# Optimization experiments

Hardware: AMD Instinct MI355X
Metric: run time of the kernel (lower is better)

Reference implementation:

```python
import jax, jax.numpy as jnp
import numpy as np

H = 768
NH = 12
HD = H // NH
FF = 3072
EPS = 1e-12
SCALE = 1.0 / (HD ** 0.5)


def _ln(x, g, b):
    m = jnp.mean(x, axis=-1, keepdims=True)
    v = jnp.mean((x - m) ** 2, axis=-1, keepdims=True)
    return (x - m) * jax.lax.rsqrt(v + EPS) * g + b


def setup_inputs() -> dict:
    key = jax.random.key(0)
    ks = jax.random.split(key, 16)
    B, Q, S, T = 8, 64, 48, 128
    s = 0.02
    return {
        "q": jax.random.normal(ks[0], (B, Q, H), jnp.float32),
        "k": jax.random.normal(ks[1], (B, S, T, H), jnp.float32),
        "mask": jax.random.randint(ks[2], (B, S, T), 0, 2, jnp.int32),
        "Wq": jax.random.normal(ks[3], (H, H), jnp.float32) * s,
        "Wkv": jax.random.normal(ks[4], (H, H), jnp.float32) * s,
        "Wo": jax.random.normal(ks[5], (H, H), jnp.float32) * s,
        "bo": jnp.zeros((H,), jnp.float32),
        "ln1_g": jnp.ones((H,), jnp.float32),
        "ln1_b": jnp.zeros((H,), jnp.float32),
        "W1": jax.random.normal(ks[6], (H, FF), jnp.float32) * s,
        "b1": jnp.zeros((FF,), jnp.float32),
        "W2": jax.random.normal(ks[7], (FF, H), jnp.float32) * s,
        "b2": jnp.zeros((H,), jnp.float32),
        "ln2_g": jnp.ones((H,), jnp.float32),
        "ln2_b": jnp.zeros((H,), jnp.float32),
    }


def reference(q, k, mask, Wq, Wkv, Wo, bo, ln1_g, ln1_b, W1, b1, W2, b2, ln2_g, ln2_b):
    B, Q, _ = q.shape
    _, S, T, _ = k.shape
    # projections (no bias)
    qp = (q @ Wq).reshape(B, Q, NH, HD)            # [b,q,h,d]
    kv = (k @ Wkv).reshape(B, S, T, NH, HD)        # [b,s,t,h,d]
    # broadcast-query grouped attention: softmax only over token dim t
    scores = jnp.einsum('bqhd,bsthd->bhqst', qp, kv) * SCALE
    scores = scores + mask.astype(scores.dtype)[:, None, None, :, :] * -10000.0
    alpha = jax.nn.softmax(scores, axis=-1)        # dropout is identity in eval
    res = jnp.einsum('bhqst,bsthd->bqshd', alpha, kv).reshape(B, Q, S, H)
    # BertSelfOutput with zero residual (residual=False)
    attn_out = _ln(res @ Wo + bo, ln1_g, ln1_b)    # [b,q,s,H]
    # FFN
    ffn = jax.nn.gelu(attn_out @ W1 + b1, approximate=False) @ W2 + b2
    return _ln(attn_out + ffn, ln2_g, ln2_b)
```

## Files before the change

### kernel.cpp

```cpp
#include <hip/hip_runtime.h>
#include <hip/hip_bf16.h>
#include <math.h>

#define B_ 8
#define Q_ 64
#define S_ 48
#define T_ 128
#define H_ 768
#define NH_ 12
#define HD_ 64
#define FF_ 3072

typedef float f32x4 __attribute__((ext_vector_type(4)));
typedef short s16x8 __attribute__((ext_vector_type(8)));
typedef short s16x4 __attribute__((ext_vector_type(4)));

__device__ __forceinline__ float ldT(const float* p, size_t i) { return p[i]; }
__device__ __forceinline__ float ldT(const __hip_bfloat16* p, size_t i) { return __bfloat162float(p[i]); }
__device__ __forceinline__ void stT(float* p, size_t i, float v) { p[i] = v; }
__device__ __forceinline__ void stT(__hip_bfloat16* p, size_t i, float v) { p[i] = __float2bfloat16(v); }

__device__ __forceinline__ short f2bf(float f) {
  __hip_bfloat16 h = __float2bfloat16(f);
  return *reinterpret_cast<short*>(&h);
}

__device__ __forceinline__ float gelu_f(float x) {
  float z = 1.5957691216f * (x + 0.044715f * x * x * x);
  z = fminf(z, 80.0f);
  float e = __expf(z);
  return x * e / (e + 1.0f);
}

__device__ __forceinline__ void gld_lds16(const void* g, void* l) {
  __builtin_amdgcn_global_load_lds(
      (const __attribute__((address_space(1))) void*)g,
      (__attribute__((address_space(3))) void*)l, 16, 0, 0);
}

__device__ __forceinline__ int swz_off(int row, int kc) {
  return row * 64 + ((kc ^ ((row >> 1) & 3)) << 4);
}

#define WAITV4() asm volatile("s_waitcnt vmcnt(4)" ::: "memory")
#define WAITV5() asm volatile("s_waitcnt vmcnt(5)" ::: "memory")
#define WAITV0() asm volatile("s_waitcnt vmcnt(0)" ::: "memory")
#define BARX()   do { __builtin_amdgcn_s_barrier(); asm volatile("" ::: "memory"); } while (0)

template<int KK, typename OT, bool BIAS, bool GELU>
__global__ __launch_bounds__(256) void gemm_mfma(
    const __hip_bfloat16* __restrict__ A,
    const __hip_bfloat16* __restrict__ BT,
    const float* __restrict__ bias, OT* __restrict__ C,
    int N, int nbx, int GB)
{
  constexpr int NT = KK / 32;
  static_assert(NT % 3 == 0 && NT >= 6, "KK must be multiple of 96");
  __shared__ char sm[3][16384];

  const int cpx = gridDim.x >> 3;
  const int xcd = blockIdx.x & 7;
  const int ci  = blockIdx.x >> 3;
  const int gsz = GB * nbx;
  const int g   = ci / gsz;
  const int r2  = ci - g * gsz;
  const int bn  = r2 / GB;
  const int bi  = r2 - bn * GB;
  const int bm  = xcd * (cpx / nbx) + g * GB + bi;
  const int m0 = bm * 128, n0 = bn * 128;

  const int tid = threadIdx.x;
  const int lane = tid & 63;
  const int wid = tid >> 6;
  const int wr = wid >> 1, wc = wid & 1;
  const int kcg = lane >> 4, rl = lane & 15;

  const __hip_bfloat16* pA[2];
  const __hip_bfloat16* pB[2];
  #pragma unroll
  for (int r = 0; r < 2; ++r) {
    const int c = tid + r * 256, row = c >> 2, slot = c & 3;
    const int kc = slot ^ ((row >> 1) & 3);
    pA[r] = A + (size_t)(m0 + row) * KK + kc * 8;
    pB[r] = BT + (size_t)(n0 + row) * KK + kc * 8;
  }
  auto stageT = [&](char* base, int off) {
    gld_lds16(pA[0] + off, base + tid * 16);
    gld_lds16(pA[1] + off, base + tid * 16 + 4096);
    gld_lds16(pB[0] + off, base + 8192 + tid * 16);
    gld_lds16(pB[1] + off, base + 8192 + tid * 16 + 4096);
  };

  int woffA[4], woffB[4];
  #pragma unroll
  for (int m = 0; m < 4; ++m)
    woffA[m] = swz_off(wr * 64 + m * 16 + rl, kcg);
  #pragma unroll
  for (int n = 0; n < 4; ++n)
    woffB[n] = 8192 + swz_off(wc * 64 + n * 16 + rl, kcg);

  f32x4 acc[4][4] = {};
  s16x8 af[4], bf[4];
  auto reads = [&](const char* base) {
    #pragma unroll
    for (int m = 0; m < 4; ++m) af[m] = *(const s16x8*)(base + woffA[m]);
    #pragma unroll
    for (int n = 0; n < 4; ++n) bf[n] = *(const s16x8*)(base + woffB[n]);
  };
  auto mfmas = [&]() {
    #pragma unroll
    for (int m = 0; m < 4; ++m)
      #pragma unroll
      for (int n = 0; n < 4; ++n)
        acc[m][n] = __builtin_amdgcn_mfma_f32_16x16x32_bf16(af[m], bf[n], acc[m][n], 0, 0, 0);
  };

  stageT(sm[0], 0);
  stageT(sm[1], 32);
  #pragma unroll
  for (int r = 0; r < 2; ++r) { pA[r] += 64; pB[r] += 64; }

  #pragma unroll 1
  for (int it = 0; it < NT / 3 - 1; ++it) {
    WAITV4(); BARX(); reads(sm[0]); stageT(sm[2], 0);  mfmas();
    WAITV4(); BARX(); reads(sm[1]); stageT(sm[0], 32); mfmas();
    WAITV4(); BARX(); reads(sm[2]); stageT(sm[1], 64); mfmas();
    #pragma unroll
    for (int r = 0; r < 2; ++r) { pA[r] += 96; pB[r] += 96; }
  }
  WAITV4(); BARX(); reads(sm[0]); stageT(sm[2], 0); mfmas();
  WAITV4(); BARX(); reads(sm[1]); mfmas();
  WAITV0(); BARX(); reads(sm[2]); mfmas();

  const int colb = n0 + wc * 64 + rl;
  const int rowb = m0 + wr * 64 + (lane >> 4) * 4;
  float bv[4];
  #pragma unroll
  for (int n = 0; n < 4; ++n) bv[n] = BIAS ? bias[colb + n * 16] : 0.0f;
  #pragma unroll
  for (int m = 0; m < 4; ++m) {
    #pragma unroll
    for (int r = 0; r < 4; ++r) {
      const int row = rowb + m * 16 + r;
      #pragma unroll
      for (int n = 0; n < 4; ++n) {
        float v = acc[m][n][r] + bv[n];
        if (GELU) v = gelu_f(v);
        stT(C, (size_t)row * N + colb + n * 16, v);
      }
    }
  }
}

template<int KK, typename OT, bool BIAS, bool GELU>
__global__ __launch_bounds__(256, 2) void gemm_fat(
    const __hip_bfloat16* __restrict__ A,
    const __hip_bfloat16* __restrict__ BT,
    const float* __restrict__ bias, OT* __restrict__ C,
    int N, int nbx, int GB)
{
  constexpr int NT = KK / 32;
  static_assert(NT % 3 == 0 && NT >= 6, "KK must be multiple of 96");
  __shared__ char sm[3][20480];

  const int cpx = gridDim.x >> 3;
  const int xcd = blockIdx.x & 7;
  const int ci  = blockIdx.x >> 3;
  const int gsz = GB * nbx;
  const int g   = ci / gsz;
  const int r2  = ci - g * gsz;
  const int bn  = r2 / GB;
  const int bi  = r2 - bn * GB;
  const int bm  = xcd * (cpx / nbx) + g * GB + bi;
  const int m0 = bm * 128, n0 = bn * 192;

  const int tid = threadIdx.x;
  const int lane = tid & 63;
  const int wid = tid >> 6;
  const int wm = wid >> 1;
  const int wn = wid & 1;
  const int kcg = lane >> 4, rl = lane & 15;

  const __hip_bfloat16* pA[2];
  const __hip_bfloat16* pB[3];
  #pragma unroll
  for (int r = 0; r < 2; ++r) {
    const int c = tid + r * 256, row = c >> 2, slot = c & 3;
    const int kc = slot ^ ((row >> 1) & 3);
    pA[r] = A + (size_t)(m0 + row) * KK + kc * 8;
  }
  #pragma unroll
  for (int r = 0; r < 3; ++r) {
    const int c = tid + r * 256, row = c >> 2, slot = c & 3;
    const int kc = slot ^ ((row >> 1) & 3);
    pB[r] = BT + (size_t)(n0 + row) * KK + kc * 8;
  }
  auto stageT = [&](char* base, int off) {
    gld_lds16(pA[0] + off, base + tid * 16);
    gld_lds16(pA[1] + off, base + tid * 16 + 4096);
    gld_lds16(pB[0] + off, base + 8192 + tid * 16);
    gld_lds16(pB[1] + off, base + 8192 + tid * 16 + 4096);
    gld_lds16(pB[2] + off, base + 8192 + tid * 16 + 8192);
  };

  int woffA[4], woffB[6];
  #pragma unroll
  for (int m = 0; m < 4; ++m)
    woffA[m] = swz_off(wm * 64 + m * 16 + rl, kcg);
  #pragma unroll
  for (int n = 0; n < 6; ++n)
    woffB[n] = 8192 + swz_off(wn * 96 + n * 16 + rl, kcg);

  f32x4 acc[4][6] = {};
  s16x8 af[4], bf[6];
  auto reads = [&](const char* base) {
    #pragma unroll
    for (int m = 0; m < 4; ++m) af[m] = *(const s16x8*)(base + woffA[m]);
    #pragma unroll
    for (int n = 0; n < 6; ++n) bf[n] = *(const s16x8*)(base + woffB[n]);
  };
  auto mfmas = [&]() {
    #pragma unroll
    for (int m = 0; m < 4; ++m)
      #pragma unroll
      for (int n = 0; n < 6; ++n)
        acc[m][n] = __builtin_amdgcn_mfma_f32_16x16x32_bf16(af[m], bf[n], acc[m][n], 0, 0, 0);
  };

  stageT(sm[0], 0);
  stageT(sm[1], 32);
  #pragma unroll
  for (int r = 0; r < 2; ++r) pA[r] += 64;
  #pragma unroll
  for (int r = 0; r < 3; ++r) pB[r] += 64;

  #pragma unroll 1
  for (int it = 0; it < NT / 3 - 1; ++it) {
    WAITV5(); BARX(); reads(sm[0]); stageT(sm[2], 0);  mfmas();
    WAITV5(); BARX(); reads(sm[1]); stageT(sm[0], 32); mfmas();
    WAITV5(); BARX(); reads(sm[2]); stageT(sm[1], 64); mfmas();
    #pragma unroll
    for (int r = 0; r < 2; ++r) pA[r] += 96;
    #pragma unroll
    for (int r = 0; r < 3; ++r) pB[r] += 96;
  }
  WAITV5(); BARX(); reads(sm[0]); stageT(sm[2], 0); mfmas();
  WAITV5(); BARX(); reads(sm[1]); mfmas();
  WAITV0(); BARX(); reads(sm[2]); mfmas();

  const int colb = n0 + wn * 96 + rl;
  const int rowb = m0 + wm * 64 + (lane >> 4) * 4;
  float bv[6];
  #pragma unroll
  for (int n = 0; n < 6; ++n) bv[n] = BIAS ? bias[colb + n * 16] : 0.0f;
  #pragma unroll
  for (int m = 0; m < 4; ++m) {
    #pragma unroll
    for (int r = 0; r < 4; ++r) {
      const int row = rowb + m * 16 + r;
      #pragma unroll
      for (int n = 0; n < 6; ++n) {
        float v = acc[m][n][r] + bv[n];
        if (GELU) v = gelu_f(v);
        stT(C, (size_t)row * N + colb + n * 16, v);
      }
    }
  }
}

template<typename OT>
__global__ __launch_bounds__(256) void gemm64(
    const float* __restrict__ A, const float* __restrict__ W,
    OT* __restrict__ C, int M, int N, int K)
{
  __shared__ float As[16][65];
  __shared__ float Ws[16][65];
  const int tid = threadIdx.x;
  const int m0 = blockIdx.y * 64;
  const int n0 = blockIdx.x * 64;
  const int tx = (tid & 15) * 4;
  const int ty = (tid >> 4) * 4;
  float acc[4][4] = {};

  for (int k0 = 0; k0 < K; k0 += 16) {
    #pragma unroll
    for (int r = 0; r < 4; ++r) {
      int idx = tid + r * 256;
      int mm = idx >> 4, kk = idx & 15;
      As[kk][mm] = A[(size_t)(m0 + mm) * K + (k0 + kk)];
    }
    #pragma unroll
    for (int r = 0; r < 4; ++r) {
      int idx = tid + r * 256;
      int kk = idx >> 6, nn = idx & 63;
      Ws[kk][nn] = W[(size_t)(k0 + kk) * N + (n0 + nn)];
    }
    __syncthreads();
    #pragma unroll
    for (int kk = 0; kk < 16; ++kk) {
      float a[4], b[4];
      #pragma unroll
      for (int i = 0; i < 4; ++i) a[i] = As[kk][ty + i];
      #pragma unroll
      for (int j = 0; j < 4; ++j) b[j] = Ws[kk][tx + j];
      #pragma unroll
      for (int i = 0; i < 4; ++i)
        #pragma unroll
        for (int j = 0; j < 4; ++j) acc[i][j] += a[i] * b[j];
    }
    __syncthreads();
  }
  #pragma unroll
  for (int i = 0; i < 4; ++i)
    #pragma unroll
    for (int j = 0; j < 4; ++j)
      stT(C, (size_t)(m0 + ty + i) * N + (n0 + tx + j), acc[i][j]);
}

__global__ __launch_bounds__(256) void transpose_cast(
    const float* __restrict__ W, __hip_bfloat16* __restrict__ WT, int K, int N)
{
  __shared__ float t[32][33];
  const int n0 = blockIdx.x * 32, k0 = blockIdx.y * 32;
  const int x = threadIdx.x & 31, y4 = (threadIdx.x >> 5) * 4;
  #pragma unroll
  for (int i = 0; i < 4; ++i)
    t[y4 + i][x] = W[(size_t)(k0 + y4 + i) * N + n0 + x];
  __syncthreads();
  #pragma unroll
  for (int i = 0; i < 4; ++i)
    WT[(size_t)(n0 + y4 + i) * K + k0 + x] = __float2bfloat16(t[x][y4 + i]);
}

__global__ __launch_bounds__(256) void cast_f32_bf16(
    const float* __restrict__ x, __hip_bfloat16* __restrict__ y, size_t n4)
{
  const size_t i = (size_t)blockIdx.x * 256 + threadIdx.x;
  if (i >= n4) return;
  const float4 v = ((const float4*)x)[i];
  __hip_bfloat16 o[4] = { __float2bfloat16(v.x), __float2bfloat16(v.y),
                          __float2bfloat16(v.z), __float2bfloat16(v.w) };
  *(ushort4*)(y + i * 4) = *(ushort4*)o;
}

__global__ __launch_bounds__(256) void attn_mfma(
    const __hip_bfloat16* __restrict__ qp,
    const __hip_bfloat16* __restrict__ kvp,
    const int* __restrict__ mask,
    __hip_bfloat16* __restrict__ res)
{
  const int s = blockIdx.x, h = blockIdx.y, b = blockIdx.z;
  __shared__ __align__(16) char lds[66048];
  char* Ks = lds;
  char* VT = lds + 16384;
  char* SC = lds + 32768;
  float* mv = (float*)(lds + 65536);

  const int tid = threadIdx.x;
  const int lane = tid & 63;
  const int wid = tid >> 6;
  const int wr = wid >> 1, wc = wid & 1;
  const int kcg = lane >> 4, rl = lane & 15;

  if (tid < 128) mv[tid] = (float)mask[((size_t)b * S_ + s) * T_ + tid] * -10000.0f;

  {
    const __hip_bfloat16* qb = qp + ((size_t)b * Q_) * H_ + h * HD_;
    #pragma unroll
    for (int r = 0; r < 2; ++r) {
      const int c = tid + r * 256;
      const int qq = c >> 3, sc = c & 7;
      const int kc8 = sc ^ (qq & 7);
      gld_lds16(qb + (size_t)qq * H_ + kc8 * 8, SC + c * 16);
    }
  }
  {
    const int kc8 = tid & 7, tg = tid >> 3;
    const int t0 = tg * 4;
    const __hip_bfloat16* kb = kvp + (((size_t)b * S_ + s) * T_) * H_ + h * HD_ + kc8 * 8;
    s16x8 r0 = *(const s16x8*)(kb + (size_t)(t0 + 0) * H_);
    s16x8 r1 = *(const s16x8*)(kb + (size_t)(t0 + 1) * H_);
    s16x8 r2 = *(const s16x8*)(kb + (size_t)(t0 + 2) * H_);
    s16x8 r3 = *(const s16x8*)(kb + (size_t)(t0 + 3) * H_);
    *(s16x8*)(Ks + (t0 + 0) * 128 + ((kc8 ^ ((t0 + 0) & 7)) << 4)) = r0;
    *(s16x8*)(Ks + (t0 + 1) * 128 + ((kc8 ^ ((t0 + 1) & 7)) << 4)) = r1;
    *(s16x8*)(Ks + (t0 + 2) * 128 + ((kc8 ^ ((t0 + 2) & 7)) << 4)) = r2;
    *(s16x8*)(Ks + (t0 + 3) * 128 + ((kc8 ^ ((t0 + 3) & 7)) << 4)) = r3;
    const int tc = tg >> 1;
    const int toff = (tg & 1) * 8;
    #pragma unroll
    for (int j = 0; j < 8; ++j) {
      s16x4 v4 = { r0[j], r1[j], r2[j], r3[j] };
      const int d = kc8 * 8 + j;
      *(s16x4*)(VT + d * 256 + ((tc ^ (d & 15)) << 4) + toff) = v4;
    }
  }
  __syncthreads();

  f32x4 acc[2][4] = {};
  {
    s16x8 af[2][2], bf[2][4];
    #pragma unroll
    for (int kk = 0; kk < 2; ++kk) {
      #pragma unroll
      for (int m = 0; m < 2; ++m) {
        const int q = wr * 32 + m * 16 + rl;
        const int kc8 = kk * 4 + kcg;
        af[kk][m] = *(const s16x8*)(SC + q * 128 + ((kc8 ^ (q & 7)) << 4));
      }
      #pragma unroll
      for (int n = 0; n < 4; ++n) {
        const int t = wc * 64 + n * 16 + rl;
        const int kc8 = kk * 4 + kcg;
        bf[kk][n] = *(const s16x8*)(Ks + t * 128 + ((kc8 ^ (t & 7)) << 4));
      }
    }
    #pragma unroll
    for (int kk = 0; kk < 2; ++kk)
      #pragma unroll
      for (int m = 0; m < 2; ++m)
        #pragma unroll
        for (int n = 0; n < 4; ++n)
          acc[m][n] = __builtin_amdgcn_mfma_f32_16x16x32_bf16(af[kk][m], bf[kk][n], acc[m][n], 0, 0, 0);
  }
  __syncthreads();

  #pragma unroll
  for (int m = 0; m < 2; ++m)
    #pragma unroll
    for (int n = 0; n < 4; ++n)
      #pragma unroll
      for (int r = 0; r < 4; ++r) {
        const int q = wr * 32 + m * 16 + (lane >> 4) * 4 + r;
        const int t = wc * 64 + n * 16 + rl;
        const int tc32 = t >> 2;
        *(float*)(SC + q * 512 + ((tc32 ^ (q & 31)) << 4) + (t & 3) * 4) =
            acc[m][n][r] * 0.125f + mv[t];
      }
  __syncthreads();

  {
    const int q = tid >> 2, quarter = tid & 3;
    float vals[32];
    #pragma unroll
    for (int j = 0; j < 8; ++j) {
      const int tc32 = quarter * 8 + j;
      const f32x4 c = *(const f32x4*)(SC + q * 512 + ((tc32 ^ (q & 31)) << 4));
      vals[j * 4 + 0] = c[0]; vals[j * 4 + 1] = c[1];
      vals[j * 4 + 2] = c[2]; vals[j * 4 + 3] = c[3];
    }
    float mx = -1e30f;
    #pragma unroll
    for (int i = 0; i < 32; ++i) mx = fmaxf(mx, vals[i]);
    mx = fmaxf(mx, __shfl_xor(mx, 1, 64));
    mx = fmaxf(mx, __shfl_xor(mx, 2, 64));
    float sum = 0.0f;
    #pragma unroll
    for (int i = 0; i < 32; ++i) { vals[i] = expf(vals[i] - mx); sum += vals[i]; }
    sum += __shfl_xor(sum, 1, 64);
    sum += __shfl_xor(sum, 2, 64);
    const float inv = 1.0f / sum;
    #pragma unroll
    for (int jj = 0; jj < 4; ++jj) {
      const int tcp = quarter * 4 + jj;
      s16x8 pk;
      #pragma unroll
      for (int i = 0; i < 8; ++i) pk[i] = f2bf(vals[jj * 8 + i] * inv);
      *(s16x8*)(SC + q * 512 + ((tcp ^ (q & 15)) << 4)) = pk;
    }
  }
  __syncthreads();

  f32x4 oacc[2][2] = {};
  #pragma unroll
  for (int kt = 0; kt < 4; ++kt) {
    s16x8 pa[2], vb[2];
    #pragma unroll
    for (int m = 0; m < 2; ++m) {
      const int q = wr * 32 + m * 16 + rl;
      const int tcp = kt * 4 + kcg;
      pa[m] = *(const s16x8*)(SC + q * 512 + ((tcp ^ (q & 15)) << 4));
    }
    #pragma unroll
    for (int n = 0; n < 2; ++n) {
      const int d = wc * 32 + n * 16 + rl;
      const int tc = kt * 4 + kcg;
      vb[n] = *(const s16x8*)(VT + d * 256 + ((tc ^ (d & 15)) << 4));
    }
    #pragma unroll
    for (int m = 0; m < 2; ++m)
      #pragma unroll
      for (int n = 0; n < 2; ++n)
        oacc[m][n] = __builtin_amdgcn_mfma_f32_16x16x32_bf16(pa[m], vb[n], oacc[m][n], 0, 0, 0);
  }
  #pragma unroll
  for (int m = 0; m < 2; ++m)
    #pragma unroll
    for (int n = 0; n < 2; ++n)
      #pragma unroll
      for (int r = 0; r < 4; ++r) {
        const int q = wr * 32 + m * 16 + (lane >> 4) * 4 + r;
        const int d = wc * 32 + n * 16 + rl;
        res[(((size_t)b * Q_ + q) * S_ + s) * H_ + h * HD_ + d] =
            __float2bfloat16(oacc[m][n][r]);
      }
}

template<bool ADD, typename IT, typename OT>
__global__ __launch_bounds__(256) void ln_kernel(
    const IT* __restrict__ X, const IT* __restrict__ X2,
    const float* __restrict__ g, const float* __restrict__ bta,
    OT* __restrict__ Y)
{
  const size_t row = blockIdx.x;
  const int tid = threadIdx.x;
  float v[3];
  #pragma unroll
  for (int i = 0; i < 3; ++i) {
    int c = tid + i * 256;
    v[i] = ldT(X, row * H_ + c);
    if (ADD) v[i] += ldT(X2, row * H_ + c);
  }
  float sum = v[0] + v[1] + v[2];
  #pragma unroll
  for (int off = 32; off > 0; off >>= 1) sum += __shfl_down(sum, off, 64);
  __shared__ float red[8];
  const int w = tid >> 6;
  if ((tid & 63) == 0) red[w] = sum;
  __syncthreads();
  const float mean = (red[0] + red[1] + red[2] + red[3]) * (1.0f / 768.0f);
  float vs = 0.0f;
  #pragma unroll
  for (int i = 0; i < 3; ++i) { v[i] -= mean; vs += v[i] * v[i]; }
  #pragma unroll
  for (int off = 32; off > 0; off >>= 1) vs += __shfl_down(vs, off, 64);
  if ((tid & 63) == 0) red[4 + w] = vs;
  __syncthreads();
  const float rstd = rsqrtf((red[4] + red[5] + red[6] + red[7]) * (1.0f / 768.0f) + 1e-12f);
  #pragma unroll
  for (int i = 0; i < 3; ++i) {
    int c = tid + i * 256;
    stT(Y, row * H_ + c, v[i] * rstd * g[c] + bta[c]);
  }
}

extern "C" void kernel_launch(void* const* d_in, const int* in_sizes, int n_in,
                              void* d_out, int out_size, void* d_ws, size_t ws_size,
                              hipStream_t stream) {
  const float* q    = (const float*)d_in[0];
  const float* k    = (const float*)d_in[1];
  const int*   mask = (const int*)d_in[2];
  const float* Wq   = (const float*)d_in[3];
  const float* Wkv  = (const float*)d_in[4];
  const float* Wo   = (const float*)d_in[5];
  const float* bo   = (const float*)d_in[6];
  const float* ln1g = (const float*)d_in[7];
  const float* ln1b = (const float*)d_in[8];
  const float* W1   = (const float*)d_in[9];
  const float* b1   = (const float*)d_in[10];
  const float* W2   = (const float*)d_in[11];
  const float* b2   = (const float*)d_in[12];
  const float* ln2g = (const float*)d_in[13];
  const float* ln2b = (const float*)d_in[14];
  float* out = (float*)d_out;

  const int MROWS = B_ * Q_ * S_;
  const int KVROWS = B_ * S_ * T_;

  char* ws = (char*)d_ws;
  __hip_bfloat16* kbf  = (__hip_bfloat16*)ws;
  __hip_bfloat16* apre = (__hip_bfloat16*)ws;
  __hip_bfloat16* kvp  = (__hip_bfloat16*)(ws + 75497472);
  __hip_bfloat16* ffn1 = (__hip_bfloat16*)ws;
  __hip_bfloat16* ares = (__hip_bfloat16*)(ws + 150994944);
  __hip_bfloat16* ffn2 = ares;
  __hip_bfloat16* aln  = (__hip_bfloat16*)(ws + 188743680);
  __hip_bfloat16* qp   = (__hip_bfloat16*)(ws + 226492416);
  __hip_bfloat16* WkvT = (__hip_bfloat16*)(ws + 228065280);
  __hip_bfloat16* WoT  = (__hip_bfloat16*)(ws + 229244928);
  __hip_bfloat16* W1T  = (__hip_bfloat16*)(ws + 230424576);
  __hip_bfloat16* W2T  = (__hip_bfloat16*)(ws + 235143168);

  dim3 blk(256);

  transpose_cast<<<dim3(24, 24), blk, 0, stream>>>(Wkv, WkvT, H_, H_);
  transpose_cast<<<dim3(24, 24), blk, 0, stream>>>(Wo, WoT, H_, H_);
  transpose_cast<<<dim3(96, 24), blk, 0, stream>>>(W1, W1T, H_, FF_);
  transpose_cast<<<dim3(24, 96), blk, 0, stream>>>(W2, W2T, FF_, H_);
  cast_f32_bf16<<<dim3((KVROWS * H_ / 4 + 255) / 256), blk, 0, stream>>>(
      k, kbf, (size_t)KVROWS * H_ / 4);

  gemm64<__hip_bfloat16><<<dim3(H_ / 64, 512 / 64), blk, 0, stream>>>(
      q, Wq, qp, 512, H_, H_);
  gemm_mfma<768, __hip_bfloat16, false, false>
      <<<dim3((KVROWS / 128) * (H_ / 128)), blk, 0, stream>>>(
      kbf, WkvT, nullptr, kvp, H_, H_ / 128, 6);
  attn_mfma<<<dim3(S_, NH_, B_), blk, 0, stream>>>(qp, kvp, mask, ares);
  gemm_mfma<768, __hip_bfloat16, true, false>
      <<<dim3((MROWS / 128) * (H_ / 128)), blk, 0, stream>>>(
      ares, WoT, bo, apre, H_, H_ / 128, 6);
  ln_kernel<false, __hip_bfloat16, __hip_bfloat16><<<MROWS, blk, 0, stream>>>(
      apre, nullptr, ln1g, ln1b, aln);
  gemm_fat<768, __hip_bfloat16, true, true>
      <<<dim3((MROWS / 128) * (FF_ / 192)), blk, 0, stream>>>(
      aln, W1T, b1, ffn1, FF_, FF_ / 192, 6);
  gemm_fat<3072, __hip_bfloat16, true, false>
      <<<dim3((MROWS / 128) * (H_ / 192)), blk, 0, stream>>>(
      ffn1, W2T, b2, ffn2, H_, H_ / 192, 6);
  ln_kernel<true, __hip_bfloat16, float><<<MROWS, blk, 0, stream>>>(
      aln, ffn2, ln2g, ln2b, out);
}
```

Baseline: 596.5 us.

## Use 4-stage LDS ring with register double-buffered fragments in MFMA GEMMs

Both GEMM kernels move from a 3-buffer LDS ring to a 4-buffer ring and keep two sets of A/B register fragments. LDS reads for the next k-tile are issued before the MFMAs on the current fragments, so LDS read latency can hide behind matrix math while global-to-LDS loads stay three tiles ahead. The cost is more LDS per block (4x16KB or 4x20KB) and more VGPRs, which may lower occupancy, especially for the fat kernel bounded to 2 blocks per CU.

```diff
diff --git a/kernel.cpp b/kernel.cpp
--- a/kernel.cpp
+++ b/kernel.cpp
@@ -44,19 +44,21 @@
 
 #define WAITV4() asm volatile("s_waitcnt vmcnt(4)" ::: "memory")
 #define WAITV5() asm volatile("s_waitcnt vmcnt(5)" ::: "memory")
+#define WAITV8() asm volatile("s_waitcnt vmcnt(8)" ::: "memory")
+#define WAITV10() asm volatile("s_waitcnt vmcnt(10)" ::: "memory")
 #define WAITV0() asm volatile("s_waitcnt vmcnt(0)" ::: "memory")
 #define BARX()   do { __builtin_amdgcn_s_barrier(); asm volatile("" ::: "memory"); } while (0)
 
 template<int KK, typename OT, bool BIAS, bool GELU>
-__global__ __launch_bounds__(256) void gemm_mfma(
+__global__ __launch_bounds__(256) void gemm_ra(
     const __hip_bfloat16* __restrict__ A,
     const __hip_bfloat16* __restrict__ BT,
     const float* __restrict__ bias, OT* __restrict__ C,
     int N, int nbx, int GB)
 {
   constexpr int NT = KK / 32;
-  static_assert(NT % 3 == 0 && NT >= 6, "KK must be multiple of 96");
-  __shared__ char sm[3][16384];
+  static_assert(NT % 4 == 0 && NT >= 8, "KK must be multiple of 128");
+  __shared__ char sm[4][16384];
 
   const int cpx = gridDim.x >> 3;
   const int xcd = blockIdx.x & 7;
@@ -100,37 +102,53 @@
     woffB[n] = 8192 + swz_off(wc * 64 + n * 16 + rl, kcg);
 
   f32x4 acc[4][4] = {};
-  s16x8 af[4], bf[4];
-  auto reads = [&](const char* base) {
-    #pragma unroll
-    for (int m = 0; m < 4; ++m) af[m] = *(const s16x8*)(base + woffA[m]);
-    #pragma unroll
-    for (int n = 0; n < 4; ++n) bf[n] = *(const s16x8*)(base + woffB[n]);
-  };
-  auto mfmas = [&]() {
+  s16x8 afA[4], bfA[4], afB[4], bfB[4];
+  auto readsA = [&](const char* base) {
+    #pragma unroll
+    for (int m = 0; m < 4; ++m) afA[m] = *(const s16x8*)(base + woffA[m]);
+    #pragma unroll
+    for (int n = 0; n < 4; ++n) bfA[n] = *(const s16x8*)(base + woffB[n]);
+  };
+  auto readsB = [&](const char* base) {
+    #pragma unroll
+    for (int m = 0; m < 4; ++m) afB[m] = *(const s16x8*)(base + woffA[m]);
+    #pragma unroll
+    for (int n = 0; n < 4; ++n) bfB[n] = *(const s16x8*)(base + woffB[n]);
+  };
+  auto mfmaA = [&]() {
     #pragma unroll
     for (int m = 0; m < 4; ++m)
       #pragma unroll
       for (int n = 0; n < 4; ++n)
-        acc[m][n] = __builtin_amdgcn_mfma_f32_16x16x32_bf16(af[m], bf[n], acc[m][n], 0, 0, 0);
+        acc[m][n] = __builtin_amdgcn_mfma_f32_16x16x32_bf16(afA[m], bfA[n], acc[m][n], 0, 0, 0);
+  };
+  auto mfmaB = [&]() {
+    #pragma unroll
+    for (int m = 0; m < 4; ++m)
+      #pragma unroll
+      for (int n = 0; n < 4; ++n)
+        acc[m][n] = __builtin_amdgcn_mfma_f32_16x16x32_bf16(afB[m], bfB[n], acc[m][n], 0, 0, 0);
   };
 
   stageT(sm[0], 0);
   stageT(sm[1], 32);
-  #pragma unroll
-  for (int r = 0; r < 2; ++r) { pA[r] += 64; pB[r] += 64; }
+  stageT(sm[2], 64);
+  WAITV8(); BARX();
+  readsA(sm[0]);
 
   #pragma unroll 1
-  for (int it = 0; it < NT / 3 - 1; ++it) {
-    WAITV4(); BARX(); reads(sm[0]); stageT(sm[2], 0);  mfmas();
-    WAITV4(); BARX(); reads(sm[1]); stageT(sm[0], 32); mfmas();
-    WAITV4(); BARX(); reads(sm[2]); stageT(sm[1], 64); mfmas();
-    #pragma unroll
-    for (int r = 0; r < 2; ++r) { pA[r] += 96; pB[r] += 96; }
-  }
-  WAITV4(); BARX(); reads(sm[0]); stageT(sm[2], 0); mfmas();
-  WAITV4(); BARX(); reads(sm[1]); mfmas();
-  WAITV0(); BARX(); reads(sm[2]); mfmas();
+  for (int it = 0; it < NT / 4 - 1; ++it) {
+    WAITV4(); BARX(); stageT(sm[3], 96);  readsB(sm[1]); mfmaA();
+    WAITV4(); BARX(); stageT(sm[0], 128); readsA(sm[2]); mfmaB();
+    WAITV4(); BARX(); stageT(sm[1], 160); readsB(sm[3]); mfmaA();
+    WAITV4(); BARX(); stageT(sm[2], 192); readsA(sm[0]); mfmaB();
+    #pragma unroll
+    for (int r = 0; r < 2; ++r) { pA[r] += 128; pB[r] += 128; }
+  }
+  WAITV4(); BARX(); stageT(sm[3], 96); readsB(sm[1]); mfmaA();
+  WAITV4(); BARX();                    readsA(sm[2]); mfmaB();
+  WAITV0(); BARX();                    readsB(sm[3]); mfmaA();
+                                                      mfmaB();
 
   const int colb = n0 + wc * 64 + rl;
   const int rowb = m0 + wr * 64 + (lane >> 4) * 4;
@@ -153,15 +171,15 @@
 }
 
 template<int KK, typename OT, bool BIAS, bool GELU>
-__global__ __launch_bounds__(256, 2) void gemm_fat(
+__global__ __launch_bounds__(256, 2) void gemm_fat_ra(
     const __hip_bfloat16* __restrict__ A,
     const __hip_bfloat16* __restrict__ BT,
     const float* __restrict__ bias, OT* __restrict__ C,
     int N, int nbx, int GB)
 {
   constexpr int NT = KK / 32;
-  static_assert(NT % 3 == 0 && NT >= 6, "KK must be multiple of 96");
-  __shared__ char sm[3][20480];
+  static_assert(NT % 4 == 0 && NT >= 8, "KK must be multiple of 128");
+  __shared__ char sm[4][20480];
 
   const int cpx = gridDim.x >> 3;
   const int xcd = blockIdx.x & 7;
@@ -212,41 +230,55 @@
     woffB[n] = 8192 + swz_off(wn * 96 + n * 16 + rl, kcg);
 
   f32x4 acc[4][6] = {};
-  s16x8 af[4], bf[6];
-  auto reads = [&](const char* base) {
-    #pragma unroll
-    for (int m = 0; m < 4; ++m) af[m] = *(const s16x8*)(base + woffA[m]);
-    #pragma unroll
-    for (int n = 0; n < 6; ++n) bf[n] = *(const s16x8*)(base + woffB[n]);
-  };
-  auto mfmas = [&]() {
+  s16x8 afA[4], bfA[6], afB[4], bfB[6];
+  auto readsA = [&](const char* base) {
+    #pragma unroll
+    for (int m = 0; m < 4; ++m) afA[m] = *(const s16x8*)(base + woffA[m]);
+    #pragma unroll
+    for (int n = 0; n < 6; ++n) bfA[n] = *(const s16x8*)(base + woffB[n]);
+  };
+  auto readsB = [&](const char* base) {
+    #pragma unroll
+    for (int m = 0; m < 4; ++m) afB[m] = *(const s16x8*)(base + woffA[m]);
+    #pragma unroll
+    for (int n = 0; n < 6; ++n) bfB[n] = *(const s16x8*)(base + woffB[n]);
+  };
+  auto mfmaA = [&]() {
     #pragma unroll
     for (int m = 0; m < 4; ++m)
       #pragma unroll
       for (int n = 0; n < 6; ++n)
-        acc[m][n] = __builtin_amdgcn_mfma_f32_16x16x32_bf16(af[m], bf[n], acc[m][n], 0, 0, 0);
+        acc[m][n] = __builtin_amdgcn_mfma_f32_16x16x32_bf16(afA[m], bfA[n], acc[m][n], 0, 0, 0);
+  };
+  auto mfmaB = [&]() {
+    #pragma unroll
+    for (int m = 0; m < 4; ++m)
+      #pragma unroll
+      for (int n = 0; n < 6; ++n)
+        acc[m][n] = __builtin_amdgcn_mfma_f32_16x16x32_bf16(afB[m], bfB[n], acc[m][n], 0, 0, 0);
   };
 
   stageT(sm[0], 0);
   stageT(sm[1], 32);
-  #pragma unroll
-  for (int r = 0; r < 2; ++r) pA[r] += 64;
-  #pragma unroll
-  for (int r = 0; r < 3; ++r) pB[r] += 64;
+  stageT(sm[2], 64);
+  WAITV10(); BARX();
+  readsA(sm[0]);
 
   #pragma unroll 1
-  for (int it = 0; it < NT / 3 - 1; ++it) {
-    WAITV5(); BARX(); reads(sm[0]); stageT(sm[2], 0);  mfmas();
-    WAITV5(); BARX(); reads(sm[1]); stageT(sm[0], 32); mfmas();
-    WAITV5(); BARX(); reads(sm[2]); stageT(sm[1], 64); mfmas();
-    #pragma unroll
-    for (int r = 0; r < 2; ++r) pA[r] += 96;
-    #pragma unroll
-    for (int r = 0; r < 3; ++r) pB[r] += 96;
-  }
-  WAITV5(); BARX(); reads(sm[0]); stageT(sm[2], 0); mfmas();
-  WAITV5(); BARX(); reads(sm[1]); mfmas();
-  WAITV0(); BARX(); reads(sm[2]); mfmas();
+  for (int it = 0; it < NT / 4 - 1; ++it) {
+    WAITV5(); BARX(); stageT(sm[3], 96);  readsB(sm[1]); mfmaA();
+    WAITV5(); BARX(); stageT(sm[0], 128); readsA(sm[2]); mfmaB();
+    WAITV5(); BARX(); stageT(sm[1], 160); readsB(sm[3]); mfmaA();
+    WAITV5(); BARX(); stageT(sm[2], 192); readsA(sm[0]); mfmaB();
+    #pragma unroll
+    for (int r = 0; r < 2; ++r) pA[r] += 128;
+    #pragma unroll
+    for (int r = 0; r < 3; ++r) pB[r] += 128;
+  }
+  WAITV5(); BARX(); stageT(sm[3], 96); readsB(sm[1]); mfmaA();
+  WAITV5(); BARX();                    readsA(sm[2]); mfmaB();
+  WAITV0(); BARX();                    readsB(sm[3]); mfmaA();
+                                                      mfmaB();
 
   const int colb = n0 + wn * 96 + rl;
   const int rowb = m0 + wm * 64 + (lane >> 4) * 4;
@@ -592,19 +624,19 @@
 
   gemm64<__hip_bfloat16><<<dim3(H_ / 64, 512 / 64), blk, 0, stream>>>(
       q, Wq, qp, 512, H_, H_);
-  gemm_mfma<768, __hip_bfloat16, false, false>
+  gemm_ra<768, __hip_bfloat16, false, false>
       <<<dim3((KVROWS / 128) * (H_ / 128)), blk, 0, stream>>>(
       kbf, WkvT, nullptr, kvp, H_, H_ / 128, 6);
   attn_mfma<<<dim3(S_, NH_, B_), blk, 0, stream>>>(qp, kvp, mask, ares);
-  gemm_mfma<768, __hip_bfloat16, true, false>
+  gemm_ra<768, __hip_bfloat16, true, false>
       <<<dim3((MROWS / 128) * (H_ / 128)), blk, 0, stream>>>(
       ares, WoT, bo, apre, H_, H_ / 128, 6);
   ln_kernel<false, __hip_bfloat16, __hip_bfloat16><<<MROWS, blk, 0, stream>>>(
       apre, nullptr, ln1g, ln1b, aln);
-  gemm_fat<768, __hip_bfloat16, true, true>
+  gemm_fat_ra<768, __hip_bfloat16, true, true>
       <<<dim3((MROWS / 128) * (FF_ / 192)), blk, 0, stream>>>(
       aln, W1T, b1, ffn1, FF_, FF_ / 192, 6);
-  gemm_fat<3072, __hip_bfloat16, true, false>
+  gemm_fat_ra<3072, __hip_bfloat16, true, false>
       <<<dim3((MROWS / 128) * (H_ / 192)), blk, 0, stream>>>(
       ffn1, W2T, b2, ffn2, H_, H_ / 192, 6);
   ln_kernel<true, __hip_bfloat16, float><<<MROWS, blk, 0, stream>>>(
```

After: 597.7 us. About the same (+0.2%).
